# Performance work log

Measured on AMD Instinct MI355X. Metric: run time of the kernel, lower is better.

## Reference

```python
import jax, jax.numpy as jnp
import numpy as np
from jax import lax

KEEP_PROB = 0.9
BLOCK_SIZE = 7


def setup_inputs() -> dict:
    key = jax.random.key(0)
    x = jax.random.normal(key, (64, 64, 112, 112), dtype=jnp.float32)
    return {"x": x}


def _block_mask(init_mask, k):
    # Faithful vectorized form of the nested-loop dilation:
    # original zeroes out[i-k : i+k, j-k : j+k) (exclusive upper bound) around
    # every zero in init_mask, i.e. out[a,b] = min over i in [a-k+1, a+k],
    # j in [b-k+1, b+k] of init_mask -> min-pool (erosion) with window 2k,
    # asymmetric padding (k-1, k). Padding with init value 1.0 is the identity
    # for min on a {0,1} mask.
    return lax.reduce_window(
        init_mask,
        jnp.array(1.0, init_mask.dtype),
        lax.min,
        window_dimensions=(1, 2 * k, 2 * k),
        window_strides=(1, 1, 1),
        padding=((0, 0), (k - 1, k), (k - 1, k)),
    )


def reference(x):
    B, C, H, W = x.shape
    bs = BLOCK_SIZE
    # gamma = (1-keep_prob) * H^2 / (bs^2 * (H-bs+1)^2)
    gamma = (1.0 - KEEP_PROB) * (H ** 2) / (bs ** 2 * (H - bs + 1) ** 2)
    key = jax.random.key(42)
    # bernoulli(1-gamma): 1 = keep, 0 = drop-center
    init_mask = jax.random.bernoulli(key, 1.0 - gamma, (B, H, W)).astype(x.dtype)
    mask = _block_mask(init_mask, bs // 2)  # [B, H, W]
    out = x * mask[:, None, :, :]
    # renormalize: * (B*H*W) / sum(out)  (matches original, sums over all elems)
    out = out * (B * H * W) / jnp.sum(out)
    return out
```

## Files before the change

### kernel.cpp

```cpp
#include <hip/hip_runtime.h>
#include <stdint.h>

#define B_      64
#define H_      112
#define W_      112
#define HW_     12544
#define CHW_    802816
#define NV4_    12845056
#define NSUMBLK 2048

typedef float v4f __attribute__((ext_vector_type(4)));

__device__ __forceinline__ uint32_t rotl32(uint32_t x, int d) {
  return (x << d) | (x >> (32 - d));
}

__device__ __forceinline__ uint32_t threefry_bits(uint32_t i) {
  const uint32_t k0 = 0u, k1 = 42u;
  const uint32_t k2 = k0 ^ k1 ^ 0x1BD11BDAu;
  uint32_t x0 = 0u, x1 = i;
  x0 += k0; x1 += k1;
#define TF_R(r) { x0 += x1; x1 = rotl32(x1, (r)); x1 ^= x0; }
  TF_R(13) TF_R(15) TF_R(26) TF_R(6)
  x0 += k1; x1 += k2 + 1u;
  TF_R(17) TF_R(29) TF_R(16) TF_R(24)
  x0 += k2; x1 += k0 + 2u;
  TF_R(13) TF_R(15) TF_R(26) TF_R(6)
  x0 += k0; x1 += k1 + 3u;
  TF_R(17) TF_R(29) TF_R(16) TF_R(24)
  x0 += k1; x1 += k2 + 4u;
  TF_R(13) TF_R(15) TF_R(26) TF_R(6)
  x0 += k2; x1 += k0 + 5u;
#undef TF_R
  return x0 ^ x1;
}

__global__ __launch_bounds__(1024) void k_mask(uint8_t* __restrict__ mask,
                                               float p) {
  __shared__ uint8_t t0[HW_];
  __shared__ uint8_t t1[HW_];
  const int b = blockIdx.x;
  const int tid = threadIdx.x;
  for (int c = tid; c < HW_; c += 1024) {
    uint32_t bits = threefry_bits((uint32_t)(b * HW_ + c));
    float u = __uint_as_float((bits >> 9) | 0x3f800000u) - 1.0f;
    t0[c] = (u < p) ? (uint8_t)1 : (uint8_t)0;
  }
  __syncthreads();
  for (int c = tid; c < HW_; c += 1024) {
    int a = c / W_, j = c - a * W_;
    int lo = a - 2; if (lo < 0) lo = 0;
    int hi = a + 3; if (hi > H_ - 1) hi = H_ - 1;
    unsigned v = 1u;
    for (int i = lo; i <= hi; ++i) v &= t0[i * W_ + j];
    t1[c] = (uint8_t)v;
  }
  __syncthreads();
  for (int c = tid; c < HW_; c += 1024) {
    int a = c / W_, j = c - a * W_;
    int lo = j - 2; if (lo < 0) lo = 0;
    int hi = j + 3; if (hi > W_ - 1) hi = W_ - 1;
    unsigned v = 1u;
    for (int jj = lo; jj <= hi; ++jj) v &= t1[a * W_ + jj];
    mask[b * HW_ + c] = (uint8_t)v;
  }
}

__global__ __launch_bounds__(256) void k_sum(const float4* __restrict__ x4,
                                             const uint8_t* __restrict__ mask,
                                             float* __restrict__ partials) {
  float acc = 0.0f;
  const int stride = NSUMBLK * 256;
  for (int f = blockIdx.x * 256 + threadIdx.x; f < NV4_; f += stride) {
    float4 v = x4[f];
    int e = f << 2;
    int b = e / CHW_;
    int hw = (e - b * CHW_) % HW_;
    uint32_t mw = *(const uint32_t*)(mask + b * HW_ + hw);
    acc += (mw & 0x000000ffu) ? v.x : 0.0f;
    acc += (mw & 0x0000ff00u) ? v.y : 0.0f;
    acc += (mw & 0x00ff0000u) ? v.z : 0.0f;
    acc += (mw & 0xff000000u) ? v.w : 0.0f;
  }
  for (int off = 32; off > 0; off >>= 1)
    acc += __shfl_down(acc, off, 64);
  __shared__ float part[4];
  if ((threadIdx.x & 63) == 0) part[threadIdx.x >> 6] = acc;
  __syncthreads();
  if (threadIdx.x == 0)
    partials[blockIdx.x] = part[0] + part[1] + part[2] + part[3];
}

__global__ __launch_bounds__(256) void k_fin(const float* __restrict__ partials,
                                             float* __restrict__ scale) {
  double acc = 0.0;
  for (int i = threadIdx.x; i < NSUMBLK; i += 256)
    acc += (double)partials[i];
  for (int off = 32; off > 0; off >>= 1)
    acc += __shfl_down(acc, off, 64);
  __shared__ double part[4];
  if ((threadIdx.x & 63) == 0) part[threadIdx.x >> 6] = acc;
  __syncthreads();
  if (threadIdx.x == 0) {
    double s = part[0] + part[1] + part[2] + part[3];
    *scale = (float)(802816.0 / s);
  }
}

__global__ __launch_bounds__(256) void k_scale(const float4* __restrict__ x4,
                                               const uint8_t* __restrict__ mask,
                                               const float* __restrict__ scalep,
                                               v4f* __restrict__ out4) {
  const float scale = *scalep;
  const int stride = gridDim.x * 256;
  for (int f = blockIdx.x * 256 + threadIdx.x; f < NV4_; f += stride) {
    float4 v = x4[f];
    int e = f << 2;
    int b = e / CHW_;
    int hw = (e - b * CHW_) % HW_;
    uint32_t mw = *(const uint32_t*)(mask + b * HW_ + hw);
    v4f o;
    o.x = (mw & 0x000000ffu) ? v.x * scale : 0.0f;
    o.y = (mw & 0x0000ff00u) ? v.y * scale : 0.0f;
    o.z = (mw & 0x00ff0000u) ? v.z * scale : 0.0f;
    o.w = (mw & 0xff000000u) ? v.w * scale : 0.0f;
    __builtin_nontemporal_store(o, &out4[f]);
  }
}

extern "C" void kernel_launch(void* const* d_in, const int* in_sizes, int n_in,
                              void* d_out, int out_size, void* d_ws, size_t ws_size,
                              hipStream_t stream) {
  const float* x = (const float*)d_in[0];
  float* out = (float*)d_out;
  char* ws = (char*)d_ws;
  float* scale = (float*)ws;
  float* partials = (float*)(ws + 16);
  uint8_t* mask = (uint8_t*)(ws + 16384);

  double gamma = (1.0 - 0.9) * 12544.0 / 550564.0;
  float p = (float)(1.0 - gamma);

  k_mask <<<B_,      1024, 0, stream>>>(mask, p);
  k_sum  <<<NSUMBLK, 256,  0, stream>>>((const float4*)x, mask, partials);
  k_fin  <<<1,       256,  0, stream>>>(partials, scale);
  k_scale<<<8192,    256,  0, stream>>>((const float4*)x, mask, scale,
                                        (v4f*)out);
}
```

Baseline: 392.7 us.

## Tile mask generation by row strips, remove index divisions, fold final reduction into scale

The mask kernel is split into 4-row strips per block with halo rows recomputed, which raises block count from 64 to 1792 at the cost of redundant RNG work on halo rows. The sum and scale kernels use a 2D grid indexed by batch and channel, so the per-element div/mod on flat indices goes away and each mask word is reused across 4 channels in the sum. The separate finalize kernel is removed. Every scale block now reduces the 1024 partials itself, which drops one launch but repeats a small reduction in 4096 blocks.

```diff
diff --git a/kernel.cpp b/kernel.cpp
--- a/kernel.cpp
+++ b/kernel.cpp
@@ -2,12 +2,13 @@
 #include <stdint.h>
 
 #define B_      64
+#define C_      64
 #define H_      112
 #define W_      112
 #define HW_     12544
-#define CHW_    802816
-#define NV4_    12845056
-#define NSUMBLK 2048
+#define HW4_    3136
+#define CHW4_   200704
+#define NPART   1024
 
 typedef float v4f __attribute__((ext_vector_type(4)));
 
@@ -35,52 +36,67 @@
   return x0 ^ x1;
 }
 
-__global__ __launch_bounds__(1024) void k_mask(uint8_t* __restrict__ mask,
-                                               float p) {
-  __shared__ uint8_t t0[HW_];
-  __shared__ uint8_t t1[HW_];
-  const int b = blockIdx.x;
+__global__ __launch_bounds__(256) void k_mask(uint8_t* __restrict__ mask,
+                                              float p) {
+  __shared__ uint8_t t0[9 * W_];
+  __shared__ uint8_t t1[4 * W_];
+  const int b = blockIdx.y;
+  const int r0 = blockIdx.x << 2;
   const int tid = threadIdx.x;
-  for (int c = tid; c < HW_; c += 1024) {
-    uint32_t bits = threefry_bits((uint32_t)(b * HW_ + c));
-    float u = __uint_as_float((bits >> 9) | 0x3f800000u) - 1.0f;
-    t0[c] = (u < p) ? (uint8_t)1 : (uint8_t)0;
+  for (int i = tid; i < 9 * W_; i += 256) {
+    int row = i / W_;
+    int j = i - row * W_;
+    int r = r0 - 2 + row;
+    uint8_t v = 1;
+    if (r >= 0 && r < H_) {
+      uint32_t bits = threefry_bits((uint32_t)(b * HW_ + r * W_ + j));
+      float u = __uint_as_float((bits >> 9) | 0x3f800000u) - 1.0f;
+      v = (u < p) ? (uint8_t)1 : (uint8_t)0;
+    }
+    t0[i] = v;
   }
   __syncthreads();
-  for (int c = tid; c < HW_; c += 1024) {
-    int a = c / W_, j = c - a * W_;
-    int lo = a - 2; if (lo < 0) lo = 0;
-    int hi = a + 3; if (hi > H_ - 1) hi = H_ - 1;
-    unsigned v = 1u;
-    for (int i = lo; i <= hi; ++i) v &= t0[i * W_ + j];
-    t1[c] = (uint8_t)v;
+  for (int i = tid; i < 4 * W_; i += 256) {
+    int row = i / W_;
+    int j = i - row * W_;
+    unsigned v = t0[row * W_ + j];
+    v &= t0[(row + 1) * W_ + j];
+    v &= t0[(row + 2) * W_ + j];
+    v &= t0[(row + 3) * W_ + j];
+    v &= t0[(row + 4) * W_ + j];
+    v &= t0[(row + 5) * W_ + j];
+    t1[i] = (uint8_t)v;
   }
   __syncthreads();
-  for (int c = tid; c < HW_; c += 1024) {
-    int a = c / W_, j = c - a * W_;
+  for (int i = tid; i < 4 * W_; i += 256) {
+    int row = i / W_;
+    int j = i - row * W_;
     int lo = j - 2; if (lo < 0) lo = 0;
     int hi = j + 3; if (hi > W_ - 1) hi = W_ - 1;
     unsigned v = 1u;
-    for (int jj = lo; jj <= hi; ++jj) v &= t1[a * W_ + jj];
-    mask[b * HW_ + c] = (uint8_t)v;
+    for (int jj = lo; jj <= hi; ++jj) v &= t1[row * W_ + jj];
+    mask[b * HW_ + (r0 + row) * W_ + j] = (uint8_t)v;
   }
 }
 
 __global__ __launch_bounds__(256) void k_sum(const float4* __restrict__ x4,
                                              const uint8_t* __restrict__ mask,
                                              float* __restrict__ partials) {
+  const int b = blockIdx.y;
+  const int cg = blockIdx.x;
+  const float4* xp = x4 + (size_t)b * CHW4_ + (size_t)(cg * 4) * HW4_;
+  const uint32_t* m32 = (const uint32_t*)(mask + b * HW_);
   float acc = 0.0f;
-  const int stride = NSUMBLK * 256;
-  for (int f = blockIdx.x * 256 + threadIdx.x; f < NV4_; f += stride) {
-    float4 v = x4[f];
-    int e = f << 2;
-    int b = e / CHW_;
-    int hw = (e - b * CHW_) % HW_;
-    uint32_t mw = *(const uint32_t*)(mask + b * HW_ + hw);
-    acc += (mw & 0x000000ffu) ? v.x : 0.0f;
-    acc += (mw & 0x0000ff00u) ? v.y : 0.0f;
-    acc += (mw & 0x00ff0000u) ? v.z : 0.0f;
-    acc += (mw & 0xff000000u) ? v.w : 0.0f;
+  for (int hw4 = threadIdx.x; hw4 < HW4_; hw4 += 256) {
+    uint32_t mw = m32[hw4];
+#pragma unroll
+    for (int c = 0; c < 4; ++c) {
+      float4 v = xp[c * HW4_ + hw4];
+      acc += (mw & 0x000000ffu) ? v.x : 0.0f;
+      acc += (mw & 0x0000ff00u) ? v.y : 0.0f;
+      acc += (mw & 0x00ff0000u) ? v.z : 0.0f;
+      acc += (mw & 0xff000000u) ? v.w : 0.0f;
+    }
   }
   for (int off = 32; off > 0; off >>= 1)
     acc += __shfl_down(acc, off, 64);
@@ -88,43 +104,44 @@
   if ((threadIdx.x & 63) == 0) part[threadIdx.x >> 6] = acc;
   __syncthreads();
   if (threadIdx.x == 0)
-    partials[blockIdx.x] = part[0] + part[1] + part[2] + part[3];
-}
-
-__global__ __launch_bounds__(256) void k_fin(const float* __restrict__ partials,
-                                             float* __restrict__ scale) {
-  double acc = 0.0;
-  for (int i = threadIdx.x; i < NSUMBLK; i += 256)
-    acc += (double)partials[i];
-  for (int off = 32; off > 0; off >>= 1)
-    acc += __shfl_down(acc, off, 64);
-  __shared__ double part[4];
-  if ((threadIdx.x & 63) == 0) part[threadIdx.x >> 6] = acc;
-  __syncthreads();
-  if (threadIdx.x == 0) {
-    double s = part[0] + part[1] + part[2] + part[3];
-    *scale = (float)(802816.0 / s);
-  }
+    partials[b * 16 + cg] = part[0] + part[1] + part[2] + part[3];
 }
 
 __global__ __launch_bounds__(256) void k_scale(const float4* __restrict__ x4,
                                                const uint8_t* __restrict__ mask,
-                                               const float* __restrict__ scalep,
+                                               const float* __restrict__ partials,
                                                v4f* __restrict__ out4) {
-  const float scale = *scalep;
-  const int stride = gridDim.x * 256;
-  for (int f = blockIdx.x * 256 + threadIdx.x; f < NV4_; f += stride) {
-    float4 v = x4[f];
-    int e = f << 2;
-    int b = e / CHW_;
-    int hw = (e - b * CHW_) % HW_;
-    uint32_t mw = *(const uint32_t*)(mask + b * HW_ + hw);
+  __shared__ float sscale;
+  {
+    double a = 0.0;
+    for (int i = threadIdx.x; i < NPART; i += 256)
+      a += (double)partials[i];
+    for (int off = 32; off > 0; off >>= 1)
+      a += __shfl_down(a, off, 64);
+    __shared__ double dp[4];
+    if ((threadIdx.x & 63) == 0) dp[threadIdx.x >> 6] = a;
+    __syncthreads();
+    if (threadIdx.x == 0) {
+      double s = dp[0] + dp[1] + dp[2] + dp[3];
+      sscale = (float)(802816.0 / s);
+    }
+    __syncthreads();
+  }
+  const float scale = sscale;
+  const int b = blockIdx.y;
+  const size_t base = (size_t)b * CHW4_ + (size_t)blockIdx.x * HW4_;
+  const float4* xp = x4 + base;
+  v4f* op = out4 + base;
+  const uint32_t* m32 = (const uint32_t*)(mask + b * HW_);
+  for (int hw4 = threadIdx.x; hw4 < HW4_; hw4 += 256) {
+    uint32_t mw = m32[hw4];
+    float4 v = xp[hw4];
     v4f o;
     o.x = (mw & 0x000000ffu) ? v.x * scale : 0.0f;
     o.y = (mw & 0x0000ff00u) ? v.y * scale : 0.0f;
     o.z = (mw & 0x00ff0000u) ? v.z * scale : 0.0f;
     o.w = (mw & 0xff000000u) ? v.w * scale : 0.0f;
-    __builtin_nontemporal_store(o, &out4[f]);
+    __builtin_nontemporal_store(o, &op[hw4]);
   }
 }
 
@@ -134,16 +151,14 @@
   const float* x = (const float*)d_in[0];
   float* out = (float*)d_out;
   char* ws = (char*)d_ws;
-  float* scale = (float*)ws;
   float* partials = (float*)(ws + 16);
   uint8_t* mask = (uint8_t*)(ws + 16384);
 
   double gamma = (1.0 - 0.9) * 12544.0 / 550564.0;
   float p = (float)(1.0 - gamma);
 
-  k_mask <<<B_,      1024, 0, stream>>>(mask, p);
-  k_sum  <<<NSUMBLK, 256,  0, stream>>>((const float4*)x, mask, partials);
-  k_fin  <<<1,       256,  0, stream>>>(partials, scale);
-  k_scale<<<8192,    256,  0, stream>>>((const float4*)x, mask, scale,
-                                        (v4f*)out);
+  k_mask <<<dim3(28, 64), 256, 0, stream>>>(mask, p);
+  k_sum  <<<dim3(16, 64), 256, 0, stream>>>((const float4*)x, mask, partials);
+  k_scale<<<dim3(64, 64), 256, 0, stream>>>((const float4*)x, mask, partials,
+                                            (v4f*)out);
 }
```

Result: faster. 382.4 us (-2.6%).
